# Performance work log

Hardware: AMD Instinct MI355X
Metric: run time of the kernel (lower is better)

Reference implementation:

```python
import jax, jax.numpy as jnp
import numpy as np
import math

N = 10000      # nodes (batched protein residues)
E = 160000     # edges (avg degree 16)
D = 1280       # node/hidden dim (ESM2-650M)
M = 24         # message_dim
EE = 16        # edge_embedding_dim (sinusoidal distance features)
L = 6          # num EGNN layers
LN_EPS = 1e-5


def setup_inputs() -> dict:
    key = jax.random.key(0)
    ks = jax.random.split(key, 20)
    s = 0.02
    h = jax.random.normal(ks[0], (N, D), jnp.float32)
    pos = jax.random.normal(ks[1], (N, 3), jnp.float32) * 10.0
    edge_index = jax.random.randint(ks[2], (2, E), 0, N, jnp.int32)
    msg_in_dim = 2 * D + EE + 1  # h_i, h_j, edge_attr, radial
    params = dict(
        node_emb_W=jax.random.normal(ks[3], (D, D), jnp.float32) * s,
        node_emb_b=jnp.zeros((D,), jnp.float32),
        msg_W1=jax.random.normal(ks[4], (L, msg_in_dim, M), jnp.float32) * s,
        msg_b1=jnp.zeros((L, M), jnp.float32),
        msg_W2=jax.random.normal(ks[5], (L, M, M), jnp.float32) * s,
        msg_b2=jnp.zeros((L, M), jnp.float32),
        coord_W1=jax.random.normal(ks[6], (L - 1, M, M), jnp.float32) * s,
        coord_b1=jnp.zeros((L - 1, M), jnp.float32),
        coord_W2=jax.random.normal(ks[7], (L - 1, M, 1), jnp.float32) * s,  # no bias
        node_W1=jax.random.normal(ks[8], (L, D + M, M), jnp.float32) * s,
        node_b1=jnp.zeros((L, M), jnp.float32),
        node_W2=jax.random.normal(ks[9], (L, M, D), jnp.float32) * s,
        node_b2=jnp.zeros((L, D), jnp.float32),
        ln_g=jnp.ones((L, D), jnp.float32),
        ln_b=jnp.zeros((L, D), jnp.float32),
    )
    return dict(h=h, pos=pos, edge_index=edge_index, **params)


def reference(h, pos, edge_index, node_emb_W, node_emb_b, msg_W1, msg_b1,
              msg_W2, msg_b2, coord_W1, coord_b1, coord_W2,
              node_W1, node_b1, node_W2, node_b2, ln_g, ln_b):
    row, col = edge_index[0], edge_index[1]  # PyG: row=source j, col=target i

    # sinusoidal distance embedding from initial coordinates (computed once)
    freqs = jnp.exp(-math.log(10000.0) * jnp.arange(0, EE, 2, dtype=jnp.float32) / EE)
    d0 = pos[row] - pos[col]                      # (E,3)
    dist = jnp.sqrt(jnp.sum(d0 * d0, axis=1))     # (E,)
    ang = dist[:, None] * freqs[None, :]          # (E, EE/2)
    edge_attr = jnp.stack([jnp.sin(ang), jnp.cos(ang)], axis=2).reshape(dist.shape[0], EE)

    h = h @ node_emb_W + node_emb_b

    # mean-aggregation denominator: in-degree of target nodes, clamped to 1
    deg = jax.ops.segment_sum(jnp.ones_like(dist), col, num_segments=N)
    denom = jnp.maximum(deg, 1.0)[:, None]

    for l in range(L):
        cd = pos[row] - pos[col]                  # (E,3) coord_diff
        radial = jnp.sum(cd * cd, axis=1, keepdims=True)
        msg_in = jnp.concatenate([h[col], h[row], edge_attr, radial], axis=-1)  # (E, 2D+EE+1)
        msg = jax.nn.silu(jax.nn.silu(msg_in @ msg_W1[l] + msg_b1[l]) @ msg_W2[l] + msg_b2[l])
        msg_agg = jax.ops.segment_sum(msg, col, num_segments=N) / denom  # scatter-mean
        if l < L - 1:  # update_coords for all but last layer
            w = jax.nn.silu(msg @ coord_W1[l] + coord_b1[l]) @ coord_W2[l]  # (E,1)
            pos = pos + jax.ops.segment_sum(cd * w, col, num_segments=N)   # index_add
        h_up = jax.nn.silu(jnp.concatenate([h, msg_agg], axis=-1) @ node_W1[l] + node_b1[l]) @ node_W2[l] + node_b2[l]
        hn = h + h_up
        mu = jnp.mean(hn, axis=-1, keepdims=True)
        var = jnp.mean((hn - mu) ** 2, axis=-1, keepdims=True)
        h = (hn - mu) / jnp.sqrt(var + LN_EPS) * ln_g[l] + ln_b[l]
        # dropout is identity in eval mode
    return h, pos
```

## Files before the change

### kernel.cpp

```cpp
#include <hip/hip_runtime.h>

#define NN 10000
#define NE 160000
#define DD 1280
#define MM 24

typedef __attribute__((ext_vector_type(8))) short bf16x8;
typedef __attribute__((ext_vector_type(4))) float f32x4;
typedef unsigned short u16;

#define O_nembW 0
#define O_nembB 1638400
#define O_msgW1 1639680
#define O_msgB1 2010880
#define O_msgW2 2011136
#define O_msgB2 2014592
#define O_cW1   2014848
#define O_cB1   2017792
#define O_cW2   2017920
#define O_nW1   2018048
#define O_nB1   2205824
#define O_nW2   2206080
#define O_nB2   2390400
#define O_lnG   2398080
#define O_lnB   2405760
#define TOTW    2413440

__device__ __forceinline__ float b2f(u16 u){
  union { unsigned int i; float f; } v; v.i = ((unsigned int)u) << 16; return v.f;
}
__device__ __forceinline__ u16 f2b(float f){
  union { float f; unsigned int i; } v; v.f = f;
  return (u16)((v.i + 0x7fffu + ((v.i >> 16) & 1u)) >> 16);
}
__device__ __forceinline__ float silu_f(float x){ return x / (1.f + __expf(-x)); }

__device__ __forceinline__ void gll16(const u16* g, u16* l){
  __builtin_amdgcn_global_load_lds(
      (const __attribute__((address_space(1))) void*)g,
      (__attribute__((address_space(3))) void*)l, 16, 0, 0);
}

__global__ __launch_bounds__(256) void k_sniff(const u16* __restrict__ h0, int* __restrict__ modep)
{
  __shared__ int cnt;
  if (threadIdx.x == 0) cnt = 0;
  __syncthreads();
  int local = 0;
  for (int i = threadIdx.x; i < 16384; i += 256){
    unsigned int e = (h0[i] >> 7) & 0xFF;
    if (e >= 0xE0) local++;
  }
  atomicAdd(&cnt, local);
  __syncthreads();
  if (threadIdx.x == 0) *modep = (cnt > 16) ? 0 : 1;
}

__global__ __launch_bounds__(256) void k_cvtw(const int* __restrict__ modep,
    const void* p0, const void* p1, const void* p2, const void* p3, const void* p4,
    const void* p5, const void* p6, const void* p7, const void* p8, const void* p9,
    const void* p10, const void* p11, const void* p12, const void* p13, const void* p14,
    u16* __restrict__ wbf)
{
  int i = blockIdx.x * 256 + threadIdx.x;
  if (i >= TOTW) return;
  int mode = *modep;
  const void* src; int j; int sz;
  if      (i < O_nembB){ src = p0;  j = i - O_nembW; sz = 1638400; }
  else if (i < O_msgW1){ src = p1;  j = i - O_nembB; sz = 1280; }
  else if (i < O_msgB1){ src = p2;  j = i - O_msgW1; sz = 371088; }
  else if (i < O_msgW2){ src = p3;  j = i - O_msgB1; sz = 144; }
  else if (i < O_msgB2){ src = p4;  j = i - O_msgW2; sz = 3456; }
  else if (i < O_cW1)  { src = p5;  j = i - O_msgB2; sz = 144; }
  else if (i < O_cB1)  { src = p6;  j = i - O_cW1;   sz = 2880; }
  else if (i < O_cW2)  { src = p7;  j = i - O_cB1;   sz = 120; }
  else if (i < O_nW1)  { src = p8;  j = i - O_cW2;   sz = 120; }
  else if (i < O_nB1)  { src = p9;  j = i - O_nW1;   sz = 187776; }
  else if (i < O_nW2)  { src = p10; j = i - O_nB1;   sz = 144; }
  else if (i < O_nB2)  { src = p11; j = i - O_nW2;   sz = 184320; }
  else if (i < O_lnG)  { src = p12; j = i - O_nB2;   sz = 7680; }
  else if (i < O_lnB)  { src = p13; j = i - O_lnG;   sz = 7680; }
  else                 { src = p14; j = i - O_lnB;   sz = 7680; }
  u16 v = 0;
  if (j < sz) v = mode ? ((const u16*)src)[j] : f2b(((const float*)src)[j]);
  wbf[i] = v;
}

__global__ __launch_bounds__(256) void k_tr(const u16* __restrict__ win, u16* __restrict__ wout)
{
  __shared__ u16 tile[32][33];
  int bx = blockIdx.x % 40, by = blockIdx.x / 40;
  int tc = threadIdx.x & 31, tr = threadIdx.x >> 5;
  #pragma unroll
  for (int p = 0; p < 4; p++){
    int r = p*8 + tr;
    tile[r][tc] = win[(size_t)(by*32 + r)*1280 + bx*32 + tc];
  }
  __syncthreads();
  #pragma unroll
  for (int p = 0; p < 4; p++){
    int r = p*8 + tr;
    wout[(size_t)(bx*32 + r)*1280 + by*32 + tc] = tile[tc][r];
  }
}

__global__ __launch_bounds__(256) void k_packproj(const u16* __restrict__ wbf, u16* __restrict__ wproj)
{
  int i = blockIdx.x * 256 + threadIdx.x;
  if (i >= 6*80*1280) return;
  int l = i / (80*1280);
  int rem = i - l*80*1280;
  int n = rem / 1280;
  int k = rem - n*1280;
  u16 v = 0;
  if (n < 24)       v = wbf[O_msgW1 + (size_t)l*2577*24 + (size_t)k*24 + n];
  else if (n < 48)  v = wbf[O_msgW1 + (size_t)l*2577*24 + (size_t)(1280+k)*24 + (n-24)];
  else if (n < 72)  v = wbf[O_nW1   + (size_t)l*1304*24 + (size_t)k*24 + (n-48)];
  wproj[i] = v;
}

__global__ __launch_bounds__(256) void k_packw2(const u16* __restrict__ wbf, u16* __restrict__ wn2p)
{
  int i = blockIdx.x * 256 + threadIdx.x;
  int l = i / (1280*32); int rem = i - l*1280*32;
  int n = rem >> 5, k = rem & 31;
  wn2p[i] = (k < 24) ? wbf[O_nW2 + (size_t)l*24*1280 + (size_t)k*1280 + n] : (u16)0;
}

__global__ __launch_bounds__(256) void k_cvth(const void* h0, const int* __restrict__ modep,
                                              u16* __restrict__ h0b)
{
  int i = blockIdx.x * 256 + threadIdx.x;
  if (*modep){
    ((int4*)h0b)[i] = ((const int4*)h0)[i];
  } else {
    const float* s = (const float*)h0 + (size_t)i*8;
    bf16x8 o;
    #pragma unroll
    for (int j = 0; j < 8; j++) o[j] = (short)f2b(s[j]);
    *(bf16x8*)(h0b + (size_t)i*8) = o;
  }
}

__global__ __launch_bounds__(256) void k_setup(const void* pos0, const int* __restrict__ modep,
    float* __restrict__ deg, float* __restrict__ posf, float* __restrict__ posf0)
{
  int i = blockIdx.x * 256 + threadIdx.x;
  int mode = *modep;
  if (i < NN) deg[i] = 0.f;
  if (i < NN * 3){
    float p = mode ? b2f(((const u16*)pos0)[i]) : ((const float*)pos0)[i];
    posf[i] = p; posf0[i] = p;
  }
}

__global__ __launch_bounds__(256) void k_deg(const int* __restrict__ eidx, float* __restrict__ deg)
{
  int e = blockIdx.x * 256 + threadIdx.x;
  atomicAdd(&deg[eidx[NE + e]], 1.f);
}

__global__ __launch_bounds__(256) void k_prefix(const float* __restrict__ deg,
                                                int* __restrict__ offs, int* __restrict__ cursor)
{
  __shared__ int part[256];
  int t = threadIdx.x;
  int lo = t * 40, hi = lo + 40; if (hi > NN) hi = NN; if (lo > NN) lo = NN;
  int s = 0;
  for (int i = lo; i < hi; i++) s += (int)deg[i];
  part[t] = s;
  __syncthreads();
  for (int off = 1; off < 256; off <<= 1){
    int v = (t >= off) ? part[t - off] : 0;
    __syncthreads();
    part[t] += v;
    __syncthreads();
  }
  int run = (t == 0) ? 0 : part[t - 1];
  for (int i = lo; i < hi; i++){
    offs[i] = run;
    run += (int)deg[i];
    cursor[i] = 0;
  }
  if (t == 255) offs[NN] = run;
}

__global__ __launch_bounds__(256) void k_scatter(const int* __restrict__ eidx,
    const int* __restrict__ offs, int* __restrict__ cursor, int* __restrict__ iperm)
{
  int e = blockIdx.x * 256 + threadIdx.x;
  int cg = eidx[NE + e];
  int p = atomicAdd(&cursor[cg], 1);
  iperm[e] = offs[cg] + p;
}

__global__ __launch_bounds__(256) void k_gemm_init(const u16* __restrict__ h0b,
    const u16* __restrict__ wembT, const u16* __restrict__ wbf, u16* __restrict__ Cb)
{
  __shared__ u16 As[128*32];
  __shared__ u16 Bs[128*32];
  int bid = blockIdx.x;
  int bm = (bid & 7) + 8 * (bid / 80);
  int bn = (bid >> 3) % 10;
  if (bm >= 79) return;
  int t = threadIdx.x;
  int lane = t & 63, wv = t >> 6;
  int m0 = bm * 128, n0 = bn * 128;
  int col = lane & 15, quad = lane >> 4;
  int wm = wv & 1, wn = wv >> 1;
  f32x4 acc[4][4];
  #pragma unroll
  for (int mi = 0; mi < 4; mi++)
    #pragma unroll
    for (int ni = 0; ni < 4; ni++) acc[mi][ni] = (f32x4){0.f,0.f,0.f,0.f};

  for (int k0 = 0; k0 < DD; k0 += 32){
    #pragma unroll
    for (int is = 0; is < 2; is++){
      int flat = is*256 + t;
      int row = flat >> 2, seg = flat & 3;
      int grow = m0 + row; if (grow > NN-1) grow = NN-1;
      gll16(h0b + (size_t)grow*DD + k0 + seg*8, As + flat*8);
    }
    #pragma unroll
    for (int is = 0; is < 2; is++){
      int flat = is*256 + t;
      int row = flat >> 2, seg = flat & 3;
      gll16(wembT + (size_t)(n0 + row)*DD + k0 + seg*8, Bs + flat*8);
    }
    __builtin_amdgcn_s_waitcnt(0x0f70);
    __syncthreads();
    bf16x8 af[4], bfv[4];
    #pragma unroll
    for (int mi = 0; mi < 4; mi++)
      af[mi] = *(const bf16x8*)&As[(wm*64 + mi*16 + col)*32 + quad*8];
    #pragma unroll
    for (int ni = 0; ni < 4; ni++)
      bfv[ni] = *(const bf16x8*)&Bs[(wn*64 + ni*16 + col)*32 + quad*8];
    #pragma unroll
    for (int mi = 0; mi < 4; mi++)
      #pragma unroll
      for (int ni = 0; ni < 4; ni++)
        acc[mi][ni] = __builtin_amdgcn_mfma_f32_16x16x32_bf16(af[mi], bfv[ni], acc[mi][ni], 0, 0, 0);
    __syncthreads();
  }
  #pragma unroll
  for (int ni = 0; ni < 4; ni++){
    int cc = n0 + wn*64 + ni*16 + col;
    float bias = b2f(wbf[O_nembB + cc]);
    #pragma unroll
    for (int mi = 0; mi < 4; mi++){
      #pragma unroll
      for (int rr = 0; rr < 4; rr++){
        int row = m0 + wm*64 + mi*16 + quad*4 + rr;
        if (row < NN) Cb[(size_t)row*DD + cc] = f2b(acc[mi][ni][rr] + bias);
      }
    }
  }
}

__global__ __launch_bounds__(128) void k_gemm_proj(const u16* __restrict__ hbm,
    const u16* __restrict__ wproj, int layer,
    float* __restrict__ Ab, float* __restrict__ Bb, float* __restrict__ Mb)
{
  __shared__ u16 As[32*32];
  __shared__ u16 Bs[80*32];
  int t = threadIdx.x;
  int lane = t & 63, wv = t >> 6;
  int m0 = blockIdx.x * 32;
  int col = lane & 15, quad = lane >> 4;
  const u16* wp = wproj + (size_t)layer * 80 * 1280;
  f32x4 acc[5];
  #pragma unroll
  for (int ni = 0; ni < 5; ni++) acc[ni] = (f32x4){0.f,0.f,0.f,0.f};

  for (int k0 = 0; k0 < DD; k0 += 32){
    { int row = t >> 2, seg = t & 3;
      int grow = m0 + row; if (grow > NN-1) grow = NN-1;
      gll16(hbm + (size_t)grow*DD + k0 + seg*8, As + t*8); }
    #pragma unroll
    for (int is = 0; is < 3; is++){
      int flat = is*128 + t;
      if (flat < 320){
        int row = flat >> 2, seg = flat & 3;
        gll16(wp + (size_t)row*DD + k0 + seg*8, Bs + flat*8);
      }
    }
    __builtin_amdgcn_s_waitcnt(0x0f70);
    __syncthreads();
    bf16x8 af = *(const bf16x8*)&As[(wv*16 + col)*32 + quad*8];
    #pragma unroll
    for (int ni = 0; ni < 5; ni++){
      bf16x8 bv = *(const bf16x8*)&Bs[(ni*16 + col)*32 + quad*8];
      acc[ni] = __builtin_amdgcn_mfma_f32_16x16x32_bf16(af, bv, acc[ni], 0, 0, 0);
    }
    __syncthreads();
  }
  #pragma unroll
  for (int ni = 0; ni < 5; ni++){
    int n = ni*16 + col;
    if (n < 72){
      int rg = (n >= 48) ? 2 : (n >= 24 ? 1 : 0);
      int cc = n - rg*24;
      float* base = (rg == 0) ? Ab : (rg == 1) ? Bb : Mb;
      #pragma unroll
      for (int rr = 0; rr < 4; rr++){
        int m = m0 + wv*16 + quad*4 + rr;
        if (m < NN) base[m*24 + cc] = acc[ni][rr];
      }
    }
  }
}

__global__ __launch_bounds__(256) void k_edge(const int* __restrict__ eidx,
    const int* __restrict__ iperm,
    const float* __restrict__ posf, const float* __restrict__ posf0,
    const float* __restrict__ Ab, const float* __restrict__ Bb,
    const u16* __restrict__ wbf, int layer, int do_coord,
    u16* __restrict__ msgu, float* __restrict__ wcdbuf)
{
  __shared__ float sW1e[16*24], sWr[24], sB1[24], sW2[24*24], sB2[24];
  __shared__ float sCW1[24*24], sCB1[24], sCW2[24];
  int t = threadIdx.x;
  const u16* w1l = wbf + O_msgW1 + (size_t)layer * 2577 * 24;
  for (int i = t; i < 16*24; i += 256) sW1e[i] = b2f(w1l[2560*24 + i]);
  for (int i = t; i < 24; i += 256){
    sWr[i] = b2f(w1l[2576*24 + i]);
    sB1[i] = b2f(wbf[O_msgB1 + layer*24 + i]);
    sB2[i] = b2f(wbf[O_msgB2 + layer*24 + i]);
  }
  for (int i = t; i < 576; i += 256) sW2[i] = b2f(wbf[O_msgW2 + layer*576 + i]);
  if (do_coord){
    for (int i = t; i < 576; i += 256) sCW1[i] = b2f(wbf[O_cW1 + layer*576 + i]);
    for (int i = t; i < 24; i += 256){
      sCB1[i] = b2f(wbf[O_cB1 + layer*24 + i]);
      sCW2[i] = b2f(wbf[O_cW2 + layer*24 + i]);
    }
  }
  __syncthreads();
  int e = blockIdx.x * 256 + t;
  int r = eidx[e], cg = eidx[NE + e];
  int slot = iperm[e];
  float cdx = posf[r*3+0] - posf[cg*3+0];
  float cdy = posf[r*3+1] - posf[cg*3+1];
  float cdz = posf[r*3+2] - posf[cg*3+2];
  float radial = cdx*cdx + cdy*cdy + cdz*cdz;
  float ex = posf0[r*3+0] - posf0[cg*3+0];
  float ey = posf0[r*3+1] - posf0[cg*3+1];
  float ez = posf0[r*3+2] - posf0[cg*3+2];
  float dist = sqrtf(ex*ex + ey*ey + ez*ez);
  const float FR[8] = {1.f, 0.31622776601683794f, 0.1f, 0.03162277660168379f,
                       0.01f, 0.0031622776601683794f, 0.001f, 0.00031622776601683794f};
  float eav[16];
  #pragma unroll
  for (int j = 0; j < 8; j++){
    float ang = dist * FR[j];
    eav[2*j]   = __sinf(ang);
    eav[2*j+1] = __cosf(ang);
  }
  float acc[24];
  const float4* ap  = (const float4*)(Ab + cg * 24);
  const float4* bp4 = (const float4*)(Bb + r * 24);
  #pragma unroll
  for (int q = 0; q < 6; q++){
    float4 a4 = ap[q], b4 = bp4[q];
    acc[q*4+0] = a4.x + b4.x; acc[q*4+1] = a4.y + b4.y;
    acc[q*4+2] = a4.z + b4.z; acc[q*4+3] = a4.w + b4.w;
  }
  #pragma unroll
  for (int m = 0; m < 24; m++) acc[m] += sB1[m] + radial * sWr[m];
  #pragma unroll
  for (int k = 0; k < 16; k++){
    #pragma unroll
    for (int m = 0; m < 24; m++) acc[m] += eav[k] * sW1e[k*24 + m];
  }
  #pragma unroll
  for (int m = 0; m < 24; m++) acc[m] = silu_f(acc[m]);
  float msg[24];
  #pragma unroll
  for (int m = 0; m < 24; m++){
    float v = sB2[m];
    #pragma unroll
    for (int k = 0; k < 24; k++) v += acc[k] * sW2[k*24 + m];
    msg[m] = silu_f(v);
  }
  {
    bf16x8 v0, v1, v2;
    #pragma unroll
    for (int j = 0; j < 8; j++){
      v0[j] = (short)f2b(msg[j]);
      v1[j] = (short)f2b(msg[8+j]);
      v2[j] = (short)f2b(msg[16+j]);
    }
    u16* mp = msgu + (size_t)slot * 24;
    *(bf16x8*)(mp)      = v0;
    *(bf16x8*)(mp + 8)  = v1;
    *(bf16x8*)(mp + 16) = v2;
  }
  if (do_coord){
    float w = 0.f;
    #pragma unroll
    for (int m = 0; m < 24; m++){
      float v = sCB1[m];
      #pragma unroll
      for (int k = 0; k < 24; k++) v += msg[k] * sCW1[k*24 + m];
      w += silu_f(v) * sCW2[m];
    }
    wcdbuf[(size_t)slot*3+0] = cdx * w;
    wcdbuf[(size_t)slot*3+1] = cdy * w;
    wcdbuf[(size_t)slot*3+2] = cdz * w;
  }
}

__global__ __launch_bounds__(256) void k_agg(const int* __restrict__ offs,
    const u16* __restrict__ msgu, const float* __restrict__ wcdbuf,
    float* __restrict__ magg, float* __restrict__ posf,
    int do_coord, int writeout, void* __restrict__ outp, const int* __restrict__ modep)
{
  int wv = threadIdx.x >> 6, lane = threadIdx.x & 63;
  int n = blockIdx.x * 4 + wv;
  int base = offs[n], cnt = offs[n+1] - base;
  float sum = 0.f;
  if (lane < 48){
    int m = (lane < 24) ? lane : lane - 24;
    for (int j = (lane < 24 ? 0 : 1); j < cnt; j += 2)
      sum += b2f(msgu[(size_t)(base+j)*24 + m]);
  }
  sum += __shfl_down(sum, 24, 64);
  if (lane < 24) magg[n*24 + lane] = sum;
  if (do_coord){
    float sc = 0.f;
    if (lane < 48){
      int c = lane % 3, jj = lane / 3;
      for (int j = jj; j < cnt; j += 16)
        sc += wcdbuf[(size_t)(base+j)*3 + c];
    }
    sc += __shfl_down(sc, 24, 64);
    sc += __shfl_down(sc, 12, 64);
    sc += __shfl_down(sc, 6, 64);
    sc += __shfl_down(sc, 3, 64);
    if (lane < 3){
      float p = posf[n*3 + lane] + sc;
      posf[n*3 + lane] = p;
      if (writeout){
        if (*modep) ((u16*)outp)[(size_t)NN*DD + n*3 + lane] = f2b(p);
        else        ((float*)outp)[(size_t)NN*DD + n*3 + lane] = p;
      }
    }
  }
}

__global__ __launch_bounds__(256) void k_combine(
    float* __restrict__ Mb, const float* __restrict__ magg, const float* __restrict__ deg,
    const u16* __restrict__ wbf, const u16* __restrict__ wn2p, const u16* __restrict__ wproj,
    const int* __restrict__ modep,
    int layer, int last, int fuse,
    u16* __restrict__ hbm, void* __restrict__ outp,
    float* __restrict__ Ab, float* __restrict__ Bb)
{
  __shared__ u16 ylds[16*1288];
  __shared__ u16 midb[16*32];
  __shared__ float sW1b[576], sB1c[24], sMg[384], sMbs[384], sDeg[16];
  __shared__ float wpart[4][16][2];
  __shared__ float mrow[16][2];
  int t = threadIdx.x;
  int lane = t & 63, wv = t >> 6;
  int row0 = blockIdx.x * 16;
  const u16* w1b = wbf + O_nW1 + (size_t)layer*1304*24 + 1280*24;
  for (int i = t; i < 576; i += 256) sW1b[i] = b2f(w1b[i]);
  if (t < 24) sB1c[t] = b2f(wbf[O_nB1 + layer*24 + t]);
  if (t < 16) sDeg[t] = 1.f / fmaxf(deg[row0 + t], 1.f);
  for (int i = t; i < 384; i += 256){ sMg[i] = magg[row0*24 + i]; sMbs[i] = Mb[row0*24 + i]; }
  midb[t] = 0; midb[256 + t] = 0;
  __syncthreads();
  for (int o = t; o < 384; o += 256){
    int r = o / 24, m = o - r*24;
    float inv = sDeg[r];
    float a = sMbs[o] + sB1c[m];
    #pragma unroll
    for (int j = 0; j < 24; j++) a += sMg[r*24 + j] * inv * sW1b[j*24 + m];
    midb[r*32 + m] = f2b(silu_f(a));
  }
  __syncthreads();
  int col = lane & 15, quad = lane >> 4;
  bf16x8 af = *(const bf16x8*)&midb[col*32 + quad*8];
  int mode = *modep;
  float s1[4] = {0.f,0.f,0.f,0.f}, s2[4] = {0.f,0.f,0.f,0.f};
  float vals[20][4];
  const u16* wp2 = wn2p + (size_t)layer*1280*32;
  const u16* b2p = wbf + O_nB2 + (size_t)layer*1280;
  #pragma unroll
  for (int ti = 0; ti < 20; ti++){
    int n0 = wv*320 + ti*16;
    bf16x8 bfv = *(const bf16x8*)&wp2[(size_t)(n0+col)*32 + quad*8];
    f32x4 acc = {0.f,0.f,0.f,0.f};
    acc = __builtin_amdgcn_mfma_f32_16x16x32_bf16(af, bfv, acc, 0, 0, 0);
    float b2 = b2f(b2p[n0 + col]);
    #pragma unroll
    for (int rr = 0; rr < 4; rr++){
      int r = quad*4 + rr;
      float hn = b2f(hbm[(size_t)(row0 + r)*1280 + n0 + col]) + acc[rr] + b2;
      vals[ti][rr] = hn;
      s1[rr] += hn; s2[rr] += hn*hn;
    }
  }
  #pragma unroll
  for (int off = 1; off < 16; off <<= 1){
    #pragma unroll
    for (int rr = 0; rr < 4; rr++){
      s1[rr] += __shfl_xor(s1[rr], off, 64);
      s2[rr] += __shfl_xor(s2[rr], off, 64);
    }
  }
  if (col == 0){
    #pragma unroll
    for (int rr = 0; rr < 4; rr++){
      wpart[wv][quad*4+rr][0] = s1[rr];
      wpart[wv][quad*4+rr][1] = s2[rr];
    }
  }
  __syncthreads();
  if (t < 16){
    float S1 = wpart[0][t][0] + wpart[1][t][0] + wpart[2][t][0] + wpart[3][t][0];
    float S2 = wpart[0][t][1] + wpart[1][t][1] + wpart[2][t][1] + wpart[3][t][1];
    float mu = S1 * (1.f/1280.f);
    float var = S2 * (1.f/1280.f) - mu*mu;
    mrow[t][0] = mu;
    mrow[t][1] = rsqrtf(var + 1e-5f);
  }
  __syncthreads();
  const u16* gp = wbf + O_lnG + (size_t)layer*1280;
  const u16* bp = wbf + O_lnB + (size_t)layer*1280;
  #pragma unroll
  for (int ti = 0; ti < 20; ti++){
    int n0 = wv*320 + ti*16;
    int cc = n0 + col;
    float g  = b2f(gp[cc]);
    float bb = b2f(bp[cc]);
    #pragma unroll
    for (int rr = 0; rr < 4; rr++){
      int r = quad*4 + rr;
      u16 yb = f2b((vals[ti][rr] - mrow[r][0]) * mrow[r][1] * g + bb);
      hbm[(size_t)(row0 + r)*1280 + cc] = yb;
      if (fuse) ylds[r*1288 + cc] = yb;
      if (last){
        if (mode) ((u16*)outp)[(size_t)(row0+r)*1280 + cc] = yb;
        else      ((float*)outp)[(size_t)(row0+r)*1280 + cc] = b2f(yb);
      }
    }
  }
  if (!fuse) return;
  __syncthreads();
  const u16* wp = wproj + (size_t)(layer+1) * 80 * 1280;
  int nt1 = wv, nt2 = (wv == 0) ? 4 : -1;
  f32x4 pa = {0.f,0.f,0.f,0.f}, pb = {0.f,0.f,0.f,0.f};
  for (int k0 = 0; k0 < DD; k0 += 32){
    bf16x8 af2 = *(const bf16x8*)&ylds[col*1288 + k0 + quad*8];
    bf16x8 bv1 = *(const bf16x8*)&wp[(size_t)(nt1*16+col)*DD + k0 + quad*8];
    pa = __builtin_amdgcn_mfma_f32_16x16x32_bf16(af2, bv1, pa, 0, 0, 0);
    if (nt2 >= 0){
      bf16x8 bv2 = *(const bf16x8*)&wp[(size_t)(nt2*16+col)*DD + k0 + quad*8];
      pb = __builtin_amdgcn_mfma_f32_16x16x32_bf16(af2, bv2, pb, 0, 0, 0);
    }
  }
  #pragma unroll
  for (int pi = 0; pi < 2; pi++){
    int tile = (pi == 0) ? nt1 : nt2;
    if (tile < 0) continue;
    f32x4 acc = (pi == 0) ? pa : pb;
    int n = tile*16 + col;
    if (n < 72){
      int rg = (n >= 48) ? 2 : (n >= 24 ? 1 : 0);
      int cc = n - rg*24;
      float* base = (rg == 0) ? Ab : (rg == 1) ? Bb : Mb;
      #pragma unroll
      for (int rr = 0; rr < 4; rr++)
        base[(row0 + quad*4 + rr)*24 + cc] = acc[rr];
    }
  }
}

extern "C" void kernel_launch(void* const* d_in, const int* in_sizes, int n_in,
                              void* d_out, int out_size, void* d_ws, size_t ws_size,
                              hipStream_t stream)
{
  const void* h0    = d_in[0];
  const void* pos0  = d_in[1];
  const int*  eidx  = (const int*)d_in[2];

  char* w = (char*)d_ws;
  auto take = [&](size_t bytes)->char*{
    char* p = w; w += (bytes + 255) & ~(size_t)255; return p;
  };
  int*   modep  = (int*)  take(256);
  u16*   wbf    = (u16*)  take((size_t)TOTW * 2);
  u16*   wembT  = (u16*)  take((size_t)DD * DD * 2);
  u16*   wproj  = (u16*)  take((size_t)6 * 80 * 1280 * 2);
  u16*   wn2p   = (u16*)  take((size_t)6 * 1280 * 32 * 2);
  u16*   hbm    = (u16*)  take((size_t)NN * DD * 2);
  float* Ab     = (float*)take((size_t)NN * MM * 4);
  float* Bb     = (float*)take((size_t)NN * MM * 4);
  float* Mb     = (float*)take((size_t)NN * MM * 4);
  float* magg   = (float*)take((size_t)NN * MM * 4);
  float* deg    = (float*)take((size_t)NN * 4);
  float* posf   = (float*)take((size_t)NN * 3 * 4);
  float* posf0  = (float*)take((size_t)NN * 3 * 4);
  int*   offs   = (int*)  take((size_t)(NN + 1) * 4);
  int*   cursor = (int*)  take((size_t)NN * 4);
  int*   iperm  = (int*)  take((size_t)NE * 4);

  u16*   h0b    = (u16*)d_out;
  u16*   msgu   = (u16*)d_out;
  float* wcdbuf = (float*)((char*)d_out + (size_t)NE * 24 * 2);

  k_sniff<<<1, 256, 0, stream>>>((const u16*)h0, modep);
  k_cvtw<<<(TOTW + 255)/256, 256, 0, stream>>>(modep,
      d_in[3], d_in[4], d_in[5], d_in[6], d_in[7], d_in[8], d_in[9], d_in[10],
      d_in[11], d_in[12], d_in[13], d_in[14], d_in[15], d_in[16], d_in[17], wbf);
  k_tr<<<1600, 256, 0, stream>>>(wbf + O_nembW, wembT);
  k_packproj<<<(6*80*1280 + 255)/256, 256, 0, stream>>>(wbf, wproj);
  k_packw2<<<6*1280*32/256, 256, 0, stream>>>(wbf, wn2p);
  k_cvth<<<NN*DD/8/256, 256, 0, stream>>>(h0, modep, h0b);
  k_setup<<<(NN*3 + 255)/256, 256, 0, stream>>>(pos0, modep, deg, posf, posf0);
  k_deg<<<NE/256, 256, 0, stream>>>(eidx, deg);
  k_prefix<<<1, 256, 0, stream>>>(deg, offs, cursor);
  k_scatter<<<NE/256, 256, 0, stream>>>(eidx, offs, cursor, iperm);
  k_gemm_init<<<800, 256, 0, stream>>>(h0b, wembT, wbf, hbm);
  k_gemm_proj<<<313, 128, 0, stream>>>(hbm, wproj, 0, Ab, Bb, Mb);
  for (int l = 0; l < 6; l++){
    int dc = (l < 5) ? 1 : 0;
    k_edge<<<NE/256, 256, 0, stream>>>(eidx, iperm, posf, posf0, Ab, Bb, wbf, l, dc, msgu, wcdbuf);
    k_agg<<<2500, 256, 0, stream>>>(offs, msgu, wcdbuf, magg, posf,
                                    dc, (l == 4) ? 1 : 0, d_out, modep);
    k_combine<<<625, 256, 0, stream>>>(Mb, magg, deg, wbf, wn2p, wproj, modep,
                                       l, (l == 5) ? 1 : 0, (l < 5) ? 1 : 0,
                                       hbm, d_out, Ab, Bb);
  }
}
```

Before: 880.8 us.

## Widen GEMM K-tile with XOR swizzle and split-K the 72-wide projections

The init GEMM now loads 64-wide K tiles into LDS with an XOR swizzle to avoid bank conflicts, halving the number of barriers. The projection GEMM (standalone and fused into combine) switches to a split-K scheme where each of four waves covers a quarter of K for a 16-row block, with partial sums reduced through LDS atomics. The combine kernel also prefetches the residual rows into LDS asynchronously and reuses that buffer, swizzled, for the fused projection. The trade-off is more LDS atomic traffic and larger shared memory use per block in exchange for more parallelism and fewer global reads.

```diff
diff --git a/kernel.cpp b/kernel.cpp
--- a/kernel.cpp
+++ b/kernel.cpp
@@ -197,8 +197,8 @@
 __global__ __launch_bounds__(256) void k_gemm_init(const u16* __restrict__ h0b,
     const u16* __restrict__ wembT, const u16* __restrict__ wbf, u16* __restrict__ Cb)
 {
-  __shared__ u16 As[128*32];
-  __shared__ u16 Bs[128*32];
+  __shared__ u16 As[128*64];
+  __shared__ u16 Bs[128*64];
   int bid = blockIdx.x;
   int bm = (bid & 7) + 8 * (bid / 80);
   int bn = (bid >> 3) % 10;
@@ -214,34 +214,45 @@
     #pragma unroll
     for (int ni = 0; ni < 4; ni++) acc[mi][ni] = (f32x4){0.f,0.f,0.f,0.f};
 
-  for (int k0 = 0; k0 < DD; k0 += 32){
-    #pragma unroll
-    for (int is = 0; is < 2; is++){
+  for (int k0 = 0; k0 < DD; k0 += 64){
+    #pragma unroll
+    for (int is = 0; is < 4; is++){
       int flat = is*256 + t;
-      int row = flat >> 2, seg = flat & 3;
+      int row = flat >> 3, kcp = flat & 7;
+      int src = (kcp ^ (row & 7)) * 8;
       int grow = m0 + row; if (grow > NN-1) grow = NN-1;
-      gll16(h0b + (size_t)grow*DD + k0 + seg*8, As + flat*8);
-    }
-    #pragma unroll
-    for (int is = 0; is < 2; is++){
+      gll16(h0b + (size_t)grow*DD + k0 + src, As + flat*8);
+    }
+    #pragma unroll
+    for (int is = 0; is < 4; is++){
       int flat = is*256 + t;
-      int row = flat >> 2, seg = flat & 3;
-      gll16(wembT + (size_t)(n0 + row)*DD + k0 + seg*8, Bs + flat*8);
+      int row = flat >> 3, kcp = flat & 7;
+      int src = (kcp ^ (row & 7)) * 8;
+      gll16(wembT + (size_t)(n0 + row)*DD + k0 + src, Bs + flat*8);
     }
     __builtin_amdgcn_s_waitcnt(0x0f70);
     __syncthreads();
-    bf16x8 af[4], bfv[4];
-    #pragma unroll
-    for (int mi = 0; mi < 4; mi++)
-      af[mi] = *(const bf16x8*)&As[(wm*64 + mi*16 + col)*32 + quad*8];
-    #pragma unroll
-    for (int ni = 0; ni < 4; ni++)
-      bfv[ni] = *(const bf16x8*)&Bs[(wn*64 + ni*16 + col)*32 + quad*8];
-    #pragma unroll
-    for (int mi = 0; mi < 4; mi++)
+    #pragma unroll
+    for (int ks = 0; ks < 2; ks++){
+      bf16x8 af[4], bfv[4];
       #pragma unroll
-      for (int ni = 0; ni < 4; ni++)
-        acc[mi][ni] = __builtin_amdgcn_mfma_f32_16x16x32_bf16(af[mi], bfv[ni], acc[mi][ni], 0, 0, 0);
+      for (int mi = 0; mi < 4; mi++){
+        int row = wm*64 + mi*16 + col;
+        int ch = (ks*4 + quad) ^ (row & 7);
+        af[mi] = *(const bf16x8*)&As[row*64 + ch*8];
+      }
+      #pragma unroll
+      for (int ni = 0; ni < 4; ni++){
+        int row = wn*64 + ni*16 + col;
+        int ch = (ks*4 + quad) ^ (row & 7);
+        bfv[ni] = *(const bf16x8*)&Bs[row*64 + ch*8];
+      }
+      #pragma unroll
+      for (int mi = 0; mi < 4; mi++)
+        #pragma unroll
+        for (int ni = 0; ni < 4; ni++)
+          acc[mi][ni] = __builtin_amdgcn_mfma_f32_16x16x32_bf16(af[mi], bfv[ni], acc[mi][ni], 0, 0, 0);
+    }
     __syncthreads();
   }
   #pragma unroll
@@ -259,55 +270,44 @@
   }
 }
 
-__global__ __launch_bounds__(128) void k_gemm_proj(const u16* __restrict__ hbm,
+__global__ __launch_bounds__(256) void k_gemm_proj(const u16* __restrict__ hbm,
     const u16* __restrict__ wproj, int layer,
     float* __restrict__ Ab, float* __restrict__ Bb, float* __restrict__ Mb)
 {
-  __shared__ u16 As[32*32];
-  __shared__ u16 Bs[80*32];
+  __shared__ float paccS[80*16];
   int t = threadIdx.x;
   int lane = t & 63, wv = t >> 6;
-  int m0 = blockIdx.x * 32;
+  int m0 = blockIdx.x * 16;
   int col = lane & 15, quad = lane >> 4;
+  for (int i = t; i < 1280; i += 256) paccS[i] = 0.f;
+  __syncthreads();
   const u16* wp = wproj + (size_t)layer * 80 * 1280;
-  f32x4 acc[5];
-  #pragma unroll
-  for (int ni = 0; ni < 5; ni++) acc[ni] = (f32x4){0.f,0.f,0.f,0.f};
-
-  for (int k0 = 0; k0 < DD; k0 += 32){
-    { int row = t >> 2, seg = t & 3;
-      int grow = m0 + row; if (grow > NN-1) grow = NN-1;
-      gll16(hbm + (size_t)grow*DD + k0 + seg*8, As + t*8); }
-    #pragma unroll
-    for (int is = 0; is < 3; is++){
-      int flat = is*128 + t;
-      if (flat < 320){
-        int row = flat >> 2, seg = flat & 3;
-        gll16(wp + (size_t)row*DD + k0 + seg*8, Bs + flat*8);
-      }
-    }
-    __builtin_amdgcn_s_waitcnt(0x0f70);
-    __syncthreads();
-    bf16x8 af = *(const bf16x8*)&As[(wv*16 + col)*32 + quad*8];
+  f32x4 acc5[5];
+  #pragma unroll
+  for (int ni = 0; ni < 5; ni++) acc5[ni] = (f32x4){0.f,0.f,0.f,0.f};
+  #pragma unroll
+  for (int kk = 0; kk < 10; kk++){
+    int kb = wv*320 + kk*32;
+    bf16x8 a = *(const bf16x8*)&hbm[(size_t)(m0 + col)*DD + kb + quad*8];
     #pragma unroll
     for (int ni = 0; ni < 5; ni++){
-      bf16x8 bv = *(const bf16x8*)&Bs[(ni*16 + col)*32 + quad*8];
-      acc[ni] = __builtin_amdgcn_mfma_f32_16x16x32_bf16(af, bv, acc[ni], 0, 0, 0);
-    }
-    __syncthreads();
-  }
-  #pragma unroll
-  for (int ni = 0; ni < 5; ni++){
-    int n = ni*16 + col;
+      bf16x8 b = *(const bf16x8*)&wp[(size_t)(ni*16 + col)*DD + kb + quad*8];
+      acc5[ni] = __builtin_amdgcn_mfma_f32_16x16x32_bf16(a, b, acc5[ni], 0, 0, 0);
+    }
+  }
+  #pragma unroll
+  for (int ni = 0; ni < 5; ni++)
+    #pragma unroll
+    for (int rr = 0; rr < 4; rr++)
+      atomicAdd(&paccS[(ni*16 + col)*16 + quad*4 + rr], acc5[ni][rr]);
+  __syncthreads();
+  for (int i = t; i < 1280; i += 256){
+    int n = i >> 4, m = i & 15;
     if (n < 72){
       int rg = (n >= 48) ? 2 : (n >= 24 ? 1 : 0);
       int cc = n - rg*24;
       float* base = (rg == 0) ? Ab : (rg == 1) ? Bb : Mb;
-      #pragma unroll
-      for (int rr = 0; rr < 4; rr++){
-        int m = m0 + wv*16 + quad*4 + rr;
-        if (m < NN) base[m*24 + cc] = acc[ni][rr];
-      }
+      base[(m0 + m)*24 + cc] = paccS[i];
     }
   }
 }
@@ -458,20 +458,29 @@
     u16* __restrict__ hbm, void* __restrict__ outp,
     float* __restrict__ Ab, float* __restrict__ Bb)
 {
-  __shared__ u16 ylds[16*1288];
+  __shared__ u16 shRes[16*1280];
   __shared__ u16 midb[16*32];
   __shared__ float sW1b[576], sB1c[24], sMg[384], sMbs[384], sDeg[16];
   __shared__ float wpart[4][16][2];
   __shared__ float mrow[16][2];
+  __shared__ float paccS[80*16];
   int t = threadIdx.x;
   int lane = t & 63, wv = t >> 6;
   int row0 = blockIdx.x * 16;
+  #pragma unroll
+  for (int it = 0; it < 10; it++){
+    int flat = it*256 + t;
+    int r = flat / 160, off = (flat - r*160) * 8;
+    gll16(hbm + (size_t)(row0 + r)*1280 + off, shRes + flat*8);
+  }
   const u16* w1b = wbf + O_nW1 + (size_t)layer*1304*24 + 1280*24;
   for (int i = t; i < 576; i += 256) sW1b[i] = b2f(w1b[i]);
   if (t < 24) sB1c[t] = b2f(wbf[O_nB1 + layer*24 + t]);
   if (t < 16) sDeg[t] = 1.f / fmaxf(deg[row0 + t], 1.f);
   for (int i = t; i < 384; i += 256){ sMg[i] = magg[row0*24 + i]; sMbs[i] = Mb[row0*24 + i]; }
+  for (int i = t; i < 1280; i += 256) paccS[i] = 0.f;
   midb[t] = 0; midb[256 + t] = 0;
+  __builtin_amdgcn_s_waitcnt(0x0f70);
   __syncthreads();
   for (int o = t; o < 384; o += 256){
     int r = o / 24, m = o - r*24;
@@ -499,7 +508,7 @@
     #pragma unroll
     for (int rr = 0; rr < 4; rr++){
       int r = quad*4 + rr;
-      float hn = b2f(hbm[(size_t)(row0 + r)*1280 + n0 + col]) + acc[rr] + b2;
+      float hn = b2f(shRes[r*1280 + n0 + col]) + acc[rr] + b2;
       vals[ti][rr] = hn;
       s1[rr] += hn; s2[rr] += hn*hn;
     }
@@ -542,7 +551,10 @@
       int r = quad*4 + rr;
       u16 yb = f2b((vals[ti][rr] - mrow[r][0]) * mrow[r][1] * g + bb);
       hbm[(size_t)(row0 + r)*1280 + cc] = yb;
-      if (fuse) ylds[r*1288 + cc] = yb;
+      if (fuse){
+        int kc = cc >> 3;
+        shRes[r*1280 + (((kc ^ (r & 7)) << 3) | (cc & 7))] = yb;
+      }
       if (last){
         if (mode) ((u16*)outp)[(size_t)(row0+r)*1280 + cc] = yb;
         else      ((float*)outp)[(size_t)(row0+r)*1280 + cc] = b2f(yb);
@@ -552,30 +564,33 @@
   if (!fuse) return;
   __syncthreads();
   const u16* wp = wproj + (size_t)(layer+1) * 80 * 1280;
-  int nt1 = wv, nt2 = (wv == 0) ? 4 : -1;
-  f32x4 pa = {0.f,0.f,0.f,0.f}, pb = {0.f,0.f,0.f,0.f};
-  for (int k0 = 0; k0 < DD; k0 += 32){
-    bf16x8 af2 = *(const bf16x8*)&ylds[col*1288 + k0 + quad*8];
-    bf16x8 bv1 = *(const bf16x8*)&wp[(size_t)(nt1*16+col)*DD + k0 + quad*8];
-    pa = __builtin_amdgcn_mfma_f32_16x16x32_bf16(af2, bv1, pa, 0, 0, 0);
-    if (nt2 >= 0){
-      bf16x8 bv2 = *(const bf16x8*)&wp[(size_t)(nt2*16+col)*DD + k0 + quad*8];
-      pb = __builtin_amdgcn_mfma_f32_16x16x32_bf16(af2, bv2, pb, 0, 0, 0);
-    }
-  }
-  #pragma unroll
-  for (int pi = 0; pi < 2; pi++){
-    int tile = (pi == 0) ? nt1 : nt2;
-    if (tile < 0) continue;
-    f32x4 acc = (pi == 0) ? pa : pb;
-    int n = tile*16 + col;
+  f32x4 acc5[5];
+  #pragma unroll
+  for (int ni = 0; ni < 5; ni++) acc5[ni] = (f32x4){0.f,0.f,0.f,0.f};
+  #pragma unroll
+  for (int kk = 0; kk < 10; kk++){
+    int kb = wv*320 + kk*32;
+    int kc = (kb >> 3) + quad;
+    bf16x8 af2 = *(const bf16x8*)&shRes[col*1280 + ((kc ^ (col & 7)) << 3)];
+    #pragma unroll
+    for (int ni = 0; ni < 5; ni++){
+      bf16x8 bv = *(const bf16x8*)&wp[(size_t)(ni*16 + col)*DD + kb + quad*8];
+      acc5[ni] = __builtin_amdgcn_mfma_f32_16x16x32_bf16(af2, bv, acc5[ni], 0, 0, 0);
+    }
+  }
+  #pragma unroll
+  for (int ni = 0; ni < 5; ni++)
+    #pragma unroll
+    for (int rr = 0; rr < 4; rr++)
+      atomicAdd(&paccS[(ni*16 + col)*16 + quad*4 + rr], acc5[ni][rr]);
+  __syncthreads();
+  for (int i = t; i < 1280; i += 256){
+    int n = i >> 4, m = i & 15;
     if (n < 72){
       int rg = (n >= 48) ? 2 : (n >= 24 ? 1 : 0);
-      int cc = n - rg*24;
+      int cc2 = n - rg*24;
       float* base = (rg == 0) ? Ab : (rg == 1) ? Bb : Mb;
-      #pragma unroll
-      for (int rr = 0; rr < 4; rr++)
-        base[(row0 + quad*4 + rr)*24 + cc] = acc[rr];
+      base[(row0 + m)*24 + cc2] = paccS[i];
     }
   }
 }
@@ -626,7 +641,7 @@
   k_prefix<<<1, 256, 0, stream>>>(deg, offs, cursor);
   k_scatter<<<NE/256, 256, 0, stream>>>(eidx, offs, cursor, iperm);
   k_gemm_init<<<800, 256, 0, stream>>>(h0b, wembT, wbf, hbm);
-  k_gemm_proj<<<313, 128, 0, stream>>>(hbm, wproj, 0, Ab, Bb, Mb);
+  k_gemm_proj<<<625, 256, 0, stream>>>(hbm, wproj, 0, Ab, Bb, Mb);
   for (int l = 0; l < 6; l++){
     int dc = (l < 5) ? 1 : 0;
     k_edge<<<NE/256, 256, 0, stream>>>(eidx, iperm, posf, posf0, Ab, Bb, wbf, l, dc, msgu, wcdbuf);
```

Result: slower. 1.012 ms (+14.9%).
